# Kernel optimization log

Hardware: AMD Instinct MI355X
Metric: run time of the kernel (lower is better)

## Reference

```python
import jax, jax.numpy as jnp
import numpy as np

T, B, K = 512, 1024, 48            # time steps, batch, tagset size
START, STOP = K - 2, K - 1         # tag_to_ix[START_TAG], tag_to_ix[STOP_TAG]
NEG = -10000.0


def setup_inputs() -> dict:
    key = jax.random.key(0)
    k1, k2, k3, k4 = jax.random.split(key, 4)
    # post-tanh emission features (output of tanh(hidden2tag(...))), time-major [T,B,K]
    feats = jnp.tanh(jax.random.normal(k1, (T, B, K), dtype=jnp.float32))
    transitions = jax.random.normal(k2, (K, K), dtype=jnp.float32)
    # CRF structural constraints, same as torch init:
    transitions = transitions.at[START, :].set(NEG).at[:, STOP].set(NEG)
    tags = jax.random.randint(k3, (B, T), 0, K - 2)       # gold tags exclude START/STOP
    lengths = jax.random.randint(k4, (B,), 1, T + 1)      # valid sequence lengths
    return {"feats": feats, "transitions": transitions, "tags": tags, "lengths": lengths}


def _crf_loss(feats, transitions, tags, lengths):
    Tn, Bn, Kn = feats.shape
    mask = jnp.arange(Tn)[:, None] < lengths[None, :]            # [T,B] valid-token mask

    # ---- forward algorithm (logZ) ----
    alpha0 = jnp.full((Bn, Kn), NEG, dtype=feats.dtype).at[:, START].set(0.0)

    def step(alpha, x):
        feat_t, m_t = x                                          # [B,K], [B]
        # scores[b, next, prev] = alpha[b,prev] + trans[next,prev] + emit[b,next]
        scores = alpha[:, None, :] + transitions[None, :, :] + feat_t[:, :, None]
        new_alpha = jax.nn.logsumexp(scores, axis=2)             # [B,K]
        alpha = jnp.where(m_t[:, None], new_alpha, alpha)        # freeze finished seqs
        return alpha, None

    alpha, _ = jax.lax.scan(step, alpha0, (feats, mask))
    log_z = jax.nn.logsumexp(alpha + transitions[STOP][None, :], axis=1)  # [B]

    # ---- gold path score ----
    tags_ext = jnp.concatenate(
        [jnp.full((Bn, 1), START, dtype=tags.dtype), tags], axis=1)       # [B,T+1]
    prev_t = tags_ext[:, :-1]                                             # [B,T]
    next_t = tags_ext[:, 1:]                                              # [B,T]
    feats_bt = feats.transpose(1, 0, 2)                                   # [B,T,K]
    emit = jnp.take_along_axis(feats_bt, next_t[:, :, None], axis=2)[:, :, 0]  # [B,T]
    trans_s = transitions[next_t, prev_t]                                 # [B,T]
    gold = jnp.sum(jnp.where(mask.T, trans_s + emit, 0.0), axis=1)        # [B]
    last_tag = jnp.take_along_axis(tags_ext, lengths[:, None], axis=1)[:, 0]
    gold = gold + transitions[STOP, last_tag]

    return jnp.sum(log_z - gold)


def reference(feats, transitions, tags, lengths):
    return _crf_loss(feats, transitions, tags, lengths)
```

## Files before the change

kernel.cpp:

```cpp
#include <hip/hip_runtime.h>
#include <math.h>

#define T_LEN 512
#define B_N   1024
#define K_N   48
#define START_TAG (K_N - 2)
#define STOP_TAG  (K_N - 1)
#define NEG   -10000.0f


__device__ __forceinline__ float bcast(float v, int k) {
    return __uint_as_float(__builtin_amdgcn_readlane(__float_as_uint(v), k));
}

__device__ __forceinline__ float matvec48(const float (&E)[48], float src) {
    float a0 = 0.f, a1 = 0.f, a2 = 0.f, a3 = 0.f;
    #pragma unroll
    for (int k = 0; k < 48; k += 4) {
        a0 = fmaf(E[k + 0], bcast(src, k + 0), a0);
        a1 = fmaf(E[k + 1], bcast(src, k + 1), a1);
        a2 = fmaf(E[k + 2], bcast(src, k + 2), a2);
        a3 = fmaf(E[k + 3], bcast(src, k + 3), a3);
    }
    return (a0 + a1) + (a2 + a3);
}

__device__ __forceinline__ void renorm(float& q, float& C) {
    const float g = bcast(q, 0);
    C += __logf(g);
    q *= __builtin_amdgcn_rcpf(g);
}

template <int BWD>
__device__ __forceinline__ void run_chain(const float* __restrict__ fb,
                                          const float (&E)[48],
                                          int steps, int lm1, int lane_c,
                                          float& q, float& C)
{
    const size_t sT = (size_t)B_N * K_N;
    auto row_of = [&](int i) -> int {
        int r = BWD ? (lm1 - i) : i;
        r = (r < 0) ? 0 : r;
        r = (r > lm1) ? lm1 : r;
        return r;
    };
    auto step = [&](int t, float fv) {
        const bool on = t < steps;
        if (BWD) {
            const float u = q * __expf(fv);
            const float w = matvec48(E, u);
            q = on ? w : q;
        } else {
            const float w = matvec48(E, q);
            q = on ? w * __expf(fv) : q;
        }
    };

    float f0[8], f1[8];
    #pragma unroll
    for (int i = 0; i < 8; ++i)
        f0[i] = fb[(size_t)row_of(i) * sT + lane_c];

    const int nblk = (steps + 15) >> 4;
    #pragma unroll 1
    for (int blk = 0; blk < nblk; ++blk) {
        const int t0 = blk * 16;
        #pragma unroll
        for (int i = 0; i < 8; ++i)
            f1[i] = fb[(size_t)row_of(t0 + 8 + i) * sT + lane_c];
        #pragma unroll
        for (int i = 0; i < 8; ++i) {
            step(t0 + i, f0[i]);
            if (i == 3 || i == 7) renorm(q, C);
        }
        #pragma unroll
        for (int i = 0; i < 8; ++i)
            f0[i] = fb[(size_t)row_of(t0 + 16 + i) * sT + lane_c];
        #pragma unroll
        for (int i = 0; i < 8; ++i) {
            step(t0 + 8 + i, f1[i]);
            if (i == 3 || i == 7) renorm(q, C);
        }
    }
}

__global__ __launch_bounds__(128)
__attribute__((amdgpu_waves_per_eu(2, 2)))
void crf_fused_kernel(
    const float* __restrict__ feats,
    const float* __restrict__ trans,
    const int*   __restrict__ tags,
    const int*   __restrict__ lengths,
    float* __restrict__ out)
{
    const int b      = blockIdx.x;
    const int tid    = threadIdx.x;
    const int lane   = tid & 63;
    const int wid    = tid >> 6;
    const int len    = lengths[b];
    const int lm1    = len - 1;
    const int m      = (len + 1) >> 1;
    const int steps  = wid ? (len - m) : m;
    const int lane_c = (lane < K_N) ? lane : (K_N - 1);

    __shared__ __attribute__((aligned(16))) float sh_p[64];
    __shared__ float sh_cb;
    __shared__ float sh_gold;

    float E[48];
    if (wid == 0) {
        const float* tr = trans + lane_c * K_N;
        #pragma unroll
        for (int k = 0; k < 48; ++k) E[k] = __expf(tr[k]);
    } else {
        #pragma unroll
        for (int k = 0; k < 48; ++k) E[k] = __expf(trans[k * K_N + lane_c]);
    }

    const float* fb = feats + (size_t)b * K_N;
    const size_t sT = (size_t)B_N * K_N;

    float q, C = 0.0f;
    if (wid == 0) q = (lane == START_TAG) ? 1.0f : 0.0f;
    else          q = __expf(trans[STOP_TAG * K_N + lane_c]);

    if (wid == 0) run_chain<0>(fb, E, steps, lm1, lane_c, q, C);
    else          run_chain<1>(fb, E, steps, lm1, lane_c, q, C);
    renorm(q, C);

    if (wid == 1) {
        float gsum = 0.0f;
        for (int t = lane; t < len; t += 64) {
            int next = tags[(size_t)b * T_LEN + t];
            int prev = (t == 0) ? START_TAG : tags[(size_t)b * T_LEN + t - 1];
            gsum += trans[next * K_N + prev] + fb[(size_t)t * sT + next];
        }
        #pragma unroll
        for (int off = 32; off >= 1; off >>= 1)
            gsum += __shfl_xor(gsum, off);

        sh_p[lane] = q;
        if (lane == 0) {
            sh_cb = C;
            int last = tags[(size_t)b * T_LEN + len - 1];
            sh_gold = gsum + trans[STOP_TAG * K_N + last];
        }
    }
    __syncthreads();

    if (wid == 0) {
        float term = (lane < K_N) ? q * sh_p[lane] : 0.0f;
        #pragma unroll
        for (int off = 32; off >= 1; off >>= 1)
            term += __shfl_xor(term, off);
        if (lane == 0) {
            float log_z = C + sh_cb + __logf(term);
            atomicAdd(out, log_z - sh_gold);
        }
    }
}

extern "C" void kernel_launch(void* const* d_in, const int* in_sizes, int n_in,
                              void* d_out, int out_size, void* d_ws, size_t ws_size,
                              hipStream_t stream) {
    const float* feats   = (const float*)d_in[0];
    const float* trans   = (const float*)d_in[1];
    const int*   tags    = (const int*)d_in[2];
    const int*   lengths = (const int*)d_in[3];
    float* out = (float*)d_out;

    hipMemsetAsync(out, 0, sizeof(float) * out_size, stream);
    crf_fused_kernel<<<B_N, 128, 0, stream>>>(feats, trans, tags, lengths, out);
}
```

Baseline: 212.2 us.

## Schedule batch blocks longest-first via counting-sort permutation of lengths

Adds a single-block counting-sort kernel that orders batch indices by descending sequence length. The main kernel then maps blockIdx to the sorted batch entry, so the longest chains start first (LPT scheduling) and the tail imbalance across CUs shrinks. It also changes waves_per_eu from 2 to 1, which lets the compiler use more registers but may lower occupancy. The cost is an extra kernel launch plus a workspace buffer for the permutation.

```diff
diff --git a/kernel.cpp b/kernel.cpp
--- a/kernel.cpp
+++ b/kernel.cpp
@@ -84,16 +84,42 @@
     }
 }
 
+__global__ __launch_bounds__(1024)
+void lpt_sort_kernel(const int* __restrict__ lengths, int* __restrict__ perm)
+{
+    __shared__ int hist[512];
+    __shared__ int offs[512];
+    const int tid = threadIdx.x;
+    if (tid < 512) hist[tid] = 0;
+    __syncthreads();
+    const int len = lengths[tid];
+    const int key = 512 - len;
+    atomicAdd(&hist[key], 1);
+    __syncthreads();
+    if (tid < 512) offs[tid] = hist[tid];
+    __syncthreads();
+    for (int d = 1; d < 512; d <<= 1) {
+        int v = 0;
+        if (tid < 512 && tid >= d) v = offs[tid - d];
+        __syncthreads();
+        if (tid < 512) offs[tid] += v;
+        __syncthreads();
+    }
+    const int p = atomicSub(&offs[key], 1) - 1;
+    perm[p] = tid;
+}
+
 __global__ __launch_bounds__(128)
-__attribute__((amdgpu_waves_per_eu(2, 2)))
+__attribute__((amdgpu_waves_per_eu(1, 1)))
 void crf_fused_kernel(
     const float* __restrict__ feats,
     const float* __restrict__ trans,
     const int*   __restrict__ tags,
     const int*   __restrict__ lengths,
+    const int*   __restrict__ perm,
     float* __restrict__ out)
 {
-    const int b      = blockIdx.x;
+    const int b      = perm[blockIdx.x];
     const int tid    = threadIdx.x;
     const int lane   = tid & 63;
     const int wid    = tid >> 6;
@@ -168,7 +194,9 @@
     const int*   tags    = (const int*)d_in[2];
     const int*   lengths = (const int*)d_in[3];
     float* out = (float*)d_out;
+    int*   perm = (int*)d_ws;
 
     hipMemsetAsync(out, 0, sizeof(float) * out_size, stream);
-    crf_fused_kernel<<<B_N, 128, 0, stream>>>(feats, trans, tags, lengths, out);
-}
+    lpt_sort_kernel<<<1, B_N, 0, stream>>>(lengths, perm);
+    crf_fused_kernel<<<B_N, 128, 0, stream>>>(feats, trans, tags, lengths, perm, out);
+}
```

Result: faster. 195.4 us (-7.9%).
